# Optimization experiments

Measured on AMD Instinct MI355X. Metric: run time of the kernel, lower is better.

Reference implementation:

```python
import jax, jax.numpy as jnp
import numpy as np

N_QUBITS = 12
N_QLAYERS = 2
BATCH = 1024
DIM = 2 ** N_QUBITS


def _apply_1q(state, U, wire):
    # state: (B, 2**n) complex; U: (2,2) shared or (B,2,2) batched
    B = state.shape[0]
    s = state.reshape(B, 2 ** wire, 2, -1)
    if U.ndim == 2:
        s = jnp.einsum('ij,bajc->baic', U, s)
    else:
        s = jnp.einsum('bij,bajc->baic', U, s)
    return s.reshape(B, DIM)


def _apply_cnot(state, c, t):
    # CNOT with control c, target t on flat state (B, 2**n)
    B = state.shape[0]
    a, b = min(c, t), max(c, t)
    s = state.reshape(B, 2 ** a, 2, 2 ** (b - a - 1), 2, -1)
    ctrl_ax, tgt_ax = (2, 4) if c < t else (4, 2)
    s0 = jnp.take(s, 0, axis=ctrl_ax)
    s1 = jnp.take(s, 1, axis=ctrl_ax)
    flip_ax = tgt_ax - 1 if tgt_ax > ctrl_ax else tgt_ax
    s1 = jnp.flip(s1, axis=flip_ax)  # X on target where control==1
    return jnp.stack([s0, s1], axis=ctrl_ax).reshape(B, DIM)


def _ry_batched(theta):
    # theta: (B,) -> (B,2,2) RY(theta) matrices
    c = jnp.cos(theta * 0.5)
    s = jnp.sin(theta * 0.5)
    U = jnp.stack([jnp.stack([c, -s], -1), jnp.stack([s, c], -1)], -2)
    return U.astype(jnp.complex64)


def _rot(phi, theta, omega):
    # PennyLane Rot = RZ(omega) @ RY(theta) @ RZ(phi)
    c = jnp.cos(theta * 0.5)
    s = jnp.sin(theta * 0.5)
    em = jnp.exp(-0.5j * (phi + omega))   # e^{-i(phi+omega)/2}
    ep = jnp.exp(0.5j * (phi + omega))
    ed = jnp.exp(0.5j * (phi - omega))    # e^{ i(phi-omega)/2}
    edm = jnp.exp(-0.5j * (phi - omega))
    row0 = jnp.stack([em * c, -ed * s])
    row1 = jnp.stack([edm * s, ep * c])
    return jnp.stack([row0, row1]).astype(jnp.complex64)


def _circuit(x, weights):
    B = x.shape[0]
    state = jnp.zeros((B, DIM), jnp.complex64).at[:, 0].set(1.0)
    for l in range(N_QLAYERS):
        # AngleEmbedding: RY(x[:, q]) on each wire (data re-uploading)
        for q in range(N_QUBITS):
            state = _apply_1q(state, _ry_batched(x[:, q]), q)
        # StronglyEntanglingLayers (single layer slice): Rot per wire
        for q in range(N_QUBITS):
            w = weights[l, q]
            state = _apply_1q(state, _rot(w[0], w[1], w[2]), q)
        # range-1 CNOT ring (single-layer SEL => r = 1)
        for q in range(N_QUBITS):
            state = _apply_cnot(state, q, (q + 1) % N_QUBITS)
    probs = state.real ** 2 + state.imag ** 2  # (B, 2**n)
    outs = []
    for q in range(N_QUBITS):
        p = probs.reshape(B, 2 ** q, 2, -1)
        outs.append(jnp.sum(p[:, :, 0, :], axis=(1, 2)) - jnp.sum(p[:, :, 1, :], axis=(1, 2)))
    return jnp.stack(outs, axis=1)  # (B, n_qubits) <Z_q> expvals


def setup_inputs() -> dict:
    key = jax.random.key(0)
    k1, k2 = jax.random.split(key)
    x = jax.random.uniform(k1, (BATCH, N_QUBITS), jnp.float32, 0.0, 2.0 * np.pi)
    weights = jax.random.normal(k2, (N_QLAYERS, N_QUBITS, 3), jnp.float32)
    return {"x": x, "weights": weights}


def reference(x, weights):
    return _circuit(x, weights)
```

## Files before the change

### kernel.cpp

```cpp
#include <hip/hip_runtime.h>

#define NQ 12
#define NT 64


struct cpx { float x, y; };
__device__ __forceinline__ cpx cmul(cpx a, cpx b) {
    return { a.x * b.x - a.y * b.y, a.x * b.y + a.y * b.x };
}
__device__ __forceinline__ cpx cmulc(cpx a, cpx b) {
    return { a.x * b.x + a.y * b.y, a.y * b.x - a.x * b.y };
}
__device__ __forceinline__ cpx cadd(cpx a, cpx b) { return { a.x + b.x, a.y + b.y }; }
__device__ __forceinline__ cpx csub(cpx a, cpx b) { return { a.x - b.x, a.y - b.y }; }
__device__ __forceinline__ cpx shflc(cpx a, int lane) {
    cpx r; r.x = __shfl(a.x, lane, 64); r.y = __shfl(a.y, lane, 64); return r;
}

__global__ __launch_bounds__(NT) void qsim_kernel(
    const float* __restrict__ x,
    const float* __restrict__ w,
    float* __restrict__ out)
{
    __shared__ float fm[2][NQ][8];
    __shared__ cpx Amat[9][16], Bmat[9][16];
    __shared__ cpx gS[4][4];
    __shared__ cpx h0U[4], h0S[4], h11U[4], h11S[4];
    __shared__ cpx Rv[3][4][4];
    __shared__ cpx PBc[11][16];
    __shared__ cpx SAc[12][16];
    __shared__ float sval[48];

    const int t = threadIdx.x;
    const int b = blockIdx.x;

    if (t < 2 * NQ) {
        int l = t / NQ, q = t % NQ;
        float hy = 0.5f * x[b * NQ + q];
        float cy = cosf(hy), sy = sinf(hy);
        const float* wp = w + (l * NQ + q) * 3;
        float phi = wp[0], the = wp[1], om = wp[2];
        float c = cosf(0.5f * the), s = sinf(0.5f * the);
        float al = 0.5f * (phi + om), be = 0.5f * (phi - om);
        float ca = cosf(al), sa = sinf(al), cb = cosf(be), sb = sinf(be);
        float r00r =  ca * c, r00i = -sa * c;
        float r01r = -cb * s, r01i = -sb * s;
        float r10r =  cb * s, r10i = -sb * s;
        float r11r =  ca * c, r11i =  sa * c;
        float* m = fm[l][q];
        m[0] =  r00r * cy + r01r * sy;  m[1] =  r00i * cy + r01i * sy;
        m[2] = -r00r * sy + r01r * cy;  m[3] = -r00i * sy + r01i * cy;
        m[4] =  r10r * cy + r11r * sy;  m[5] =  r10i * cy + r11i * sy;
        m[6] = -r10r * sy + r11r * cy;  m[7] = -r10i * sy + r11i * cy;
    }
    __syncthreads();

    auto Vq = [&](int q, int bit) -> cpx {
        const float* m = &fm[0][q][bit ? 4 : 0]; return { m[0], m[1] };
    };
    auto Uq = [&](int q, int d, int c) -> cpx {
        const float* m = &fm[1][q][4 * d + 2 * c]; return { m[0], m[1] };
    };

    if (t < 16) {
        const int a = (t >> 3) & 1, ap = (t >> 2) & 1, c = (t >> 1) & 1, cp = t & 1;
        for (int q = 2; q <= 10; ++q) {
            cpx t0 = cmul(Vq(q, c ^ a),  Uq(q, 0, c));
            cpx t1 = cmul(Vq(q, c ^ a),  Uq(q, 1, c));
            cpx p0 = cmul(Vq(q, cp ^ ap), Uq(q, 0, cp));
            cpx p1 = cmul(Vq(q, cp ^ ap), Uq(q, 1, cp));
            cpx e0 = cmulc(t0, p0), e1 = cmulc(t1, p1);
            Amat[q - 2][t] = cadd(e0, e1);
            Bmat[q - 2][t] = csub(e0, e1);
        }
        const int s = a, sp = ap, cc = c, ccp = cp;
        cpx l0 = cmul(Uq(1, 0, cc),  Vq(1, cc ^ s));
        cpx l1 = cmul(Uq(1, 1, cc),  Vq(1, cc ^ s));
        cpx m0 = cmul(Uq(1, 0, ccp), Vq(1, ccp ^ sp));
        cpx m1 = cmul(Uq(1, 1, ccp), Vq(1, ccp ^ sp));
        cpx g  = csub(cmulc(l0, m0), cmulc(l1, m1));
        cpx lw = cmulc(Vq(0, s), Vq(0, sp));
        gS[2 * s + sp][2 * cc + ccp] = cmul(g, lw);
    }
    if (t < 4) {
        const int c0 = t >> 1, c0p = t & 1;
        cpx a0 = cmulc(Uq(0, 0, c0),  Uq(0, 0, c0p));
        cpx a1 = cmulc(Uq(0, 1, c0),  Uq(0, 1, c0p));
        h0U[t] = cadd(a0, a1);  h0S[t] = csub(a0, a1);
        cpx b0 = cmulc(Uq(11, 0, c0),  Uq(11, 0, c0p));
        cpx b1 = cmulc(Uq(11, 1, c0),  Uq(11, 1, c0p));
        h11U[t] = cadd(b0, b1);  h11S[t] = csub(b0, b1);
    }
    __syncthreads();

    if (t < 16) {
        const int s = (t >> 3) & 1, sp = (t >> 2) & 1, c10 = (t >> 1) & 1, c10p = t & 1;
        for (int V = 0; V < 3; ++V) {
            const cpx* h0  = (V == 1) ? h0U  : h0S;
            const cpx* h11 = (V == 0) ? h11U : h11S;
            cpx acc = { 0.f, 0.f };
            for (int c0 = 0; c0 < 2; ++c0)
                for (int c0p = 0; c0p < 2; ++c0p) {
                    cpx term = cmul(h0[2 * c0 + c0p], h11[2 * (c0 ^ s) + (c0p ^ sp)]);
                    term = cmul(term, Vq(11, c0 ^ s ^ c10));
                    term = cmulc(term, Vq(11, c0p ^ sp ^ c10p));
                    acc = cadd(acc, term);
                }
            Rv[V][2 * s + sp][2 * c10 + c10p] = acc;
        }
    }
    __syncthreads();

    if (t < 16) {
        const int R = t >> 2, C = t & 3;
        cpx cur = { (R == C) ? 1.f : 0.f, 0.f };
        PBc[1][t] = cur;
        for (int k = 2; k <= 10; ++k) {
            cpx nv = { 0.f, 0.f };
            for (int K = 0; K < 4; ++K)
                nv = cadd(nv, cmul(shflc(cur, 4 * R + K), Bmat[k - 2][4 * K + C]));
            cur = nv;
            PBc[k][t] = cur;
        }
        cur = { (R == C) ? 1.f : 0.f, 0.f };
        SAc[11][t] = cur;
        for (int k = 10; k >= 2; --k) {
            cpx nv = { 0.f, 0.f };
            for (int K = 0; K < 4; ++K)
                nv = cadd(nv, cmul(Amat[k - 2][4 * R + K], shflc(cur, 4 * K + C)));
            cur = nv;
            SAc[k][t] = cur;
        }
    }
    __syncthreads();

    if (t < 16) {
        for (int pi = t; pi < 48; pi += 16) {
            const int qq = pi >> 2, ssi = pi & 3;
            const int kk = (qq == 0 || qq == 11) ? 10 : qq;
            const int V  = (qq == 0) ? 1 : ((qq == 11) ? 2 : 0);
            cpx rowL[4], colR[4];
            for (int K = 0; K < 4; ++K) {
                cpx acc = { 0.f, 0.f };
                for (int R = 0; R < 4; ++R)
                    acc = cadd(acc, cmul(gS[ssi][R], PBc[kk][4 * R + K]));
                rowL[K] = acc;
                cpx acc2 = { 0.f, 0.f };
                for (int C = 0; C < 4; ++C)
                    acc2 = cadd(acc2, cmul(SAc[kk + 1][4 * K + C], Rv[V][ssi][C]));
                colR[K] = acc2;
            }
            cpx val = { 0.f, 0.f };
            for (int K = 0; K < 4; ++K) val = cadd(val, cmul(rowL[K], colR[K]));
            sval[pi] = val.x;
        }
    }
    __syncthreads();
    if (t < NQ)
        out[b * NQ + t] = sval[4 * t] + sval[4 * t + 1] + sval[4 * t + 2] + sval[4 * t + 3];
}

extern "C" void kernel_launch(void* const* d_in, const int* in_sizes, int n_in,
                              void* d_out, int out_size, void* d_ws, size_t ws_size,
                              hipStream_t stream) {
    int xi = 0, wi = 1;
    if (n_in >= 2 && in_sizes[1] > in_sizes[0]) { xi = 1; wi = 0; }
    const float* x = (const float*)d_in[xi];
    const float* w = (const float*)d_in[wi];
    float* out = (float*)d_out;
    const int B = in_sizes[xi] / NQ;
    qsim_kernel<<<B, NT, 0, stream>>>(x, w, out);
}
```

Measured before the change: 61.75 us.

## Process four batch elements per block using all 64 wavefront lanes

Each 64-thread block now handles four batch elements, one per 16-lane group. Before, only 16 of the 64 lanes did work in most phases. Shared arrays gain a per-element index, shuffles are offset to stay inside each lane group, and the grid shrinks by four. This cuts launched blocks and idle lanes, but it assumes the batch size divides by four and raises shared memory per block.

```diff
diff --git a/kernel.cpp b/kernel.cpp
--- a/kernel.cpp
+++ b/kernel.cpp
@@ -2,6 +2,7 @@
 
 #define NQ 12
 #define NT 64
+#define EPB 4
 
 
 struct cpx { float x, y; };
@@ -22,21 +23,26 @@
     const float* __restrict__ w,
     float* __restrict__ out)
 {
-    __shared__ float fm[2][NQ][8];
-    __shared__ cpx Amat[9][16], Bmat[9][16];
-    __shared__ cpx gS[4][4];
-    __shared__ cpx h0U[4], h0S[4], h11U[4], h11S[4];
-    __shared__ cpx Rv[3][4][4];
-    __shared__ cpx PBc[11][16];
-    __shared__ cpx SAc[12][16];
-    __shared__ float sval[48];
+    __shared__ float fm[EPB][2][NQ][8];
+    __shared__ cpx Amat[EPB][9][16], Bmat[EPB][9][16];
+    __shared__ cpx gS[EPB][4][4];
+    __shared__ cpx h0U[EPB][4], h0S[EPB][4], h11U[EPB][4], h11S[EPB][4];
+    __shared__ cpx Rv[EPB][3][4][4];
+    __shared__ cpx PBc[EPB][11][16];
+    __shared__ cpx SAc[EPB][12][16];
+    __shared__ float sval[EPB][48];
 
-    const int t = threadIdx.x;
-    const int b = blockIdx.x;
+    const int t    = threadIdx.x;
+    const int g    = t >> 4;
+    const int u    = t & 15;
+    const int base = t & 48;
+    const int b0   = blockIdx.x * EPB;
 
-    if (t < 2 * NQ) {
-        int l = t / NQ, q = t % NQ;
-        float hy = 0.5f * x[b * NQ + q];
+    for (int task = t; task < EPB * 2 * NQ; task += NT) {
+        int e = task / (2 * NQ);
+        int rem = task % (2 * NQ);
+        int l = rem / NQ, q = rem % NQ;
+        float hy = 0.5f * x[(b0 + e) * NQ + q];
         float cy = cosf(hy), sy = sinf(hy);
         const float* wp = w + (l * NQ + q) * 3;
         float phi = wp[0], the = wp[1], om = wp[2];
@@ -47,7 +53,7 @@
         float r01r = -cb * s, r01i = -sb * s;
         float r10r =  cb * s, r10i = -sb * s;
         float r11r =  ca * c, r11i =  sa * c;
-        float* m = fm[l][q];
+        float* m = fm[e][l][q];
         m[0] =  r00r * cy + r01r * sy;  m[1] =  r00i * cy + r01i * sy;
         m[2] = -r00r * sy + r01r * cy;  m[3] = -r00i * sy + r01i * cy;
         m[4] =  r10r * cy + r11r * sy;  m[5] =  r10i * cy + r11i * sy;
@@ -56,48 +62,48 @@
     __syncthreads();
 
     auto Vq = [&](int q, int bit) -> cpx {
-        const float* m = &fm[0][q][bit ? 4 : 0]; return { m[0], m[1] };
+        const float* m = &fm[g][0][q][bit ? 4 : 0]; return { m[0], m[1] };
     };
     auto Uq = [&](int q, int d, int c) -> cpx {
-        const float* m = &fm[1][q][4 * d + 2 * c]; return { m[0], m[1] };
+        const float* m = &fm[g][1][q][4 * d + 2 * c]; return { m[0], m[1] };
     };
 
-    if (t < 16) {
-        const int a = (t >> 3) & 1, ap = (t >> 2) & 1, c = (t >> 1) & 1, cp = t & 1;
+    {
+        const int a = (u >> 3) & 1, ap = (u >> 2) & 1, c = (u >> 1) & 1, cp = u & 1;
         for (int q = 2; q <= 10; ++q) {
             cpx t0 = cmul(Vq(q, c ^ a),  Uq(q, 0, c));
             cpx t1 = cmul(Vq(q, c ^ a),  Uq(q, 1, c));
             cpx p0 = cmul(Vq(q, cp ^ ap), Uq(q, 0, cp));
             cpx p1 = cmul(Vq(q, cp ^ ap), Uq(q, 1, cp));
             cpx e0 = cmulc(t0, p0), e1 = cmulc(t1, p1);
-            Amat[q - 2][t] = cadd(e0, e1);
-            Bmat[q - 2][t] = csub(e0, e1);
+            Amat[g][q - 2][u] = cadd(e0, e1);
+            Bmat[g][q - 2][u] = csub(e0, e1);
         }
         const int s = a, sp = ap, cc = c, ccp = cp;
         cpx l0 = cmul(Uq(1, 0, cc),  Vq(1, cc ^ s));
         cpx l1 = cmul(Uq(1, 1, cc),  Vq(1, cc ^ s));
         cpx m0 = cmul(Uq(1, 0, ccp), Vq(1, ccp ^ sp));
         cpx m1 = cmul(Uq(1, 1, ccp), Vq(1, ccp ^ sp));
-        cpx g  = csub(cmulc(l0, m0), cmulc(l1, m1));
+        cpx gg = csub(cmulc(l0, m0), cmulc(l1, m1));
         cpx lw = cmulc(Vq(0, s), Vq(0, sp));
-        gS[2 * s + sp][2 * cc + ccp] = cmul(g, lw);
+        gS[g][2 * s + sp][2 * cc + ccp] = cmul(gg, lw);
     }
-    if (t < 4) {
-        const int c0 = t >> 1, c0p = t & 1;
+    if (u < 4) {
+        const int c0 = u >> 1, c0p = u & 1;
         cpx a0 = cmulc(Uq(0, 0, c0),  Uq(0, 0, c0p));
         cpx a1 = cmulc(Uq(0, 1, c0),  Uq(0, 1, c0p));
-        h0U[t] = cadd(a0, a1);  h0S[t] = csub(a0, a1);
-        cpx b0 = cmulc(Uq(11, 0, c0),  Uq(11, 0, c0p));
-        cpx b1 = cmulc(Uq(11, 1, c0),  Uq(11, 1, c0p));
-        h11U[t] = cadd(b0, b1);  h11S[t] = csub(b0, b1);
+        h0U[g][u] = cadd(a0, a1);  h0S[g][u] = csub(a0, a1);
+        cpx b0v = cmulc(Uq(11, 0, c0),  Uq(11, 0, c0p));
+        cpx b1v = cmulc(Uq(11, 1, c0),  Uq(11, 1, c0p));
+        h11U[g][u] = cadd(b0v, b1v);  h11S[g][u] = csub(b0v, b1v);
     }
     __syncthreads();
 
-    if (t < 16) {
-        const int s = (t >> 3) & 1, sp = (t >> 2) & 1, c10 = (t >> 1) & 1, c10p = t & 1;
+    {
+        const int s = (u >> 3) & 1, sp = (u >> 2) & 1, c10 = (u >> 1) & 1, c10p = u & 1;
         for (int V = 0; V < 3; ++V) {
-            const cpx* h0  = (V == 1) ? h0U  : h0S;
-            const cpx* h11 = (V == 0) ? h11U : h11S;
+            const cpx* h0  = (V == 1) ? h0U[g]  : h0S[g];
+            const cpx* h11 = (V == 0) ? h11U[g] : h11S[g];
             cpx acc = { 0.f, 0.f };
             for (int c0 = 0; c0 < 2; ++c0)
                 for (int c0p = 0; c0p < 2; ++c0p) {
@@ -106,58 +112,60 @@
                     term = cmulc(term, Vq(11, c0p ^ sp ^ c10p));
                     acc = cadd(acc, term);
                 }
-            Rv[V][2 * s + sp][2 * c10 + c10p] = acc;
+            Rv[g][V][2 * s + sp][2 * c10 + c10p] = acc;
         }
     }
     __syncthreads();
 
-    if (t < 16) {
-        const int R = t >> 2, C = t & 3;
+    {
+        const int R = u >> 2, C = u & 3;
         cpx cur = { (R == C) ? 1.f : 0.f, 0.f };
-        PBc[1][t] = cur;
+        PBc[g][1][u] = cur;
         for (int k = 2; k <= 10; ++k) {
             cpx nv = { 0.f, 0.f };
             for (int K = 0; K < 4; ++K)
-                nv = cadd(nv, cmul(shflc(cur, 4 * R + K), Bmat[k - 2][4 * K + C]));
+                nv = cadd(nv, cmul(shflc(cur, base + 4 * R + K), Bmat[g][k - 2][4 * K + C]));
             cur = nv;
-            PBc[k][t] = cur;
+            PBc[g][k][u] = cur;
         }
         cur = { (R == C) ? 1.f : 0.f, 0.f };
-        SAc[11][t] = cur;
+        SAc[g][11][u] = cur;
         for (int k = 10; k >= 2; --k) {
             cpx nv = { 0.f, 0.f };
             for (int K = 0; K < 4; ++K)
-                nv = cadd(nv, cmul(Amat[k - 2][4 * R + K], shflc(cur, 4 * K + C)));
+                nv = cadd(nv, cmul(Amat[g][k - 2][4 * R + K], shflc(cur, base + 4 * K + C)));
             cur = nv;
-            SAc[k][t] = cur;
+            SAc[g][k][u] = cur;
         }
     }
     __syncthreads();
 
-    if (t < 16) {
-        for (int pi = t; pi < 48; pi += 16) {
-            const int qq = pi >> 2, ssi = pi & 3;
-            const int kk = (qq == 0 || qq == 11) ? 10 : qq;
-            const int V  = (qq == 0) ? 1 : ((qq == 11) ? 2 : 0);
-            cpx rowL[4], colR[4];
-            for (int K = 0; K < 4; ++K) {
-                cpx acc = { 0.f, 0.f };
-                for (int R = 0; R < 4; ++R)
-                    acc = cadd(acc, cmul(gS[ssi][R], PBc[kk][4 * R + K]));
-                rowL[K] = acc;
-                cpx acc2 = { 0.f, 0.f };
-                for (int C = 0; C < 4; ++C)
-                    acc2 = cadd(acc2, cmul(SAc[kk + 1][4 * K + C], Rv[V][ssi][C]));
-                colR[K] = acc2;
-            }
-            cpx val = { 0.f, 0.f };
-            for (int K = 0; K < 4; ++K) val = cadd(val, cmul(rowL[K], colR[K]));
-            sval[pi] = val.x;
+    for (int pi = u; pi < 48; pi += 16) {
+        const int qq = pi >> 2, ssi = pi & 3;
+        const int kk = (qq == 0 || qq == 11) ? 10 : qq;
+        const int V  = (qq == 0) ? 1 : ((qq == 11) ? 2 : 0);
+        cpx rowL[4], colR[4];
+        for (int K = 0; K < 4; ++K) {
+            cpx acc = { 0.f, 0.f };
+            for (int R = 0; R < 4; ++R)
+                acc = cadd(acc, cmul(gS[g][ssi][R], PBc[g][kk][4 * R + K]));
+            rowL[K] = acc;
+            cpx acc2 = { 0.f, 0.f };
+            for (int C = 0; C < 4; ++C)
+                acc2 = cadd(acc2, cmul(SAc[g][kk + 1][4 * K + C], Rv[g][V][ssi][C]));
+            colR[K] = acc2;
         }
+        cpx val = { 0.f, 0.f };
+        for (int K = 0; K < 4; ++K) val = cadd(val, cmul(rowL[K], colR[K]));
+        sval[g][pi] = val.x;
     }
     __syncthreads();
-    if (t < NQ)
-        out[b * NQ + t] = sval[4 * t] + sval[4 * t + 1] + sval[4 * t + 2] + sval[4 * t + 3];
+
+    if (t < EPB * NQ) {
+        int e = t / NQ, q = t % NQ;
+        out[(b0 + e) * NQ + q] =
+            sval[e][4 * q] + sval[e][4 * q + 1] + sval[e][4 * q + 2] + sval[e][4 * q + 3];
+    }
 }
 
 extern "C" void kernel_launch(void* const* d_in, const int* in_sizes, int n_in,
@@ -169,5 +177,5 @@
     const float* w = (const float*)d_in[wi];
     float* out = (float*)d_out;
     const int B = in_sizes[xi] / NQ;
-    qsim_kernel<<<B, NT, 0, stream>>>(x, w, out);
+    qsim_kernel<<<B / EPB, NT, 0, stream>>>(x, w, out);
 }
```

New measurement: 60.86 us. No clear change (-1.4%).
